# Kernel optimization log

Measured on AMD Instinct MI355X. Metric: run time of the kernel, lower is better.

## Reference

```python
import jax, jax.numpy as jnp
import numpy as np

N, K, CIN, COUT = 150000, 27, 32, 64
EPS = 1e-5
NEG_SLOPE = 0.01


def setup_inputs() -> dict:
    key = jax.random.key(0)
    k1, k2, k3, k4, k5, k6 = jax.random.split(key, 6)
    feats = jax.random.normal(k1, (N, CIN), dtype=jnp.float32)
    nbr = jax.random.randint(k2, (N, K), 0, N, dtype=jnp.int32)
    mask = jax.random.randint(k3, (N, K), 0, 2, dtype=jnp.int32).astype(jnp.bool_)
    # per-offset conv weights [K, Cin, Cout], kaiming-ish scale
    W = jax.random.normal(k4, (K, CIN, COUT), dtype=jnp.float32) / np.sqrt(K * CIN)
    gamma = jax.random.normal(k5, (COUT,), dtype=jnp.float32) * 0.1 + 1.0
    beta = jax.random.normal(k6, (COUT,), dtype=jnp.float32) * 0.1
    return {"feats": feats, "W": W, "gamma": gamma, "beta": beta, "nbr": nbr, "mask": mask}


def reference(feats, W, gamma, beta, nbr, mask):
    # sparse conv as gather-GEMM-(implicit scatter): out[n] = sum_k W[k]^T f[nbr[n,k]]
    gathered = jnp.where(mask[..., None], feats[nbr], 0.0)          # [N, K, Cin]
    out = jnp.einsum('nkc,kcd->nd', gathered, W)                     # [N, Cout]
    # BatchNorm over voxel axis (training-mode batch stats)
    mean = jnp.mean(out, axis=0)
    var = jnp.var(out, axis=0)
    out = (out - mean) * jax.lax.rsqrt(var + EPS) * gamma + beta
    # LeakyReLU, negative_slope = 0.01
    return jnp.where(out >= 0, out, NEG_SLOPE * out)
```

## Files before the change

### kernel.cpp

```cpp
#include <hip/hip_runtime.h>

#define N_VOX  150000
#define KNBR   27
#define CIN    32
#define COUT   64
#define NBUCKET 64
#define NEG_SLOPE 0.01f
#define EPS 1e-5f

typedef __bf16 bf16x8 __attribute__((ext_vector_type(8)));
typedef float  f32x4  __attribute__((ext_vector_type(4)));


__global__ __launch_bounds__(256) void prepack_feats(
    const float* __restrict__ f, __bf16* __restrict__ fb)
{
    const int i = blockIdx.x * 256 + threadIdx.x;
    if (i >= N_VOX * CIN / 8) return;
    const float4* p = reinterpret_cast<const float4*>(f) + (size_t)i * 2;
    const float4 a = p[0], b = p[1];
    bf16x8 o;
    o[0] = (__bf16)a.x; o[1] = (__bf16)a.y; o[2] = (__bf16)a.z; o[3] = (__bf16)a.w;
    o[4] = (__bf16)b.x; o[5] = (__bf16)b.y; o[6] = (__bf16)b.z; o[7] = (__bf16)b.w;
    reinterpret_cast<bf16x8*>(fb)[i] = o;
}

__global__ __launch_bounds__(256) void prepack_w(
    const float* __restrict__ W, __bf16* __restrict__ Wp)
{
    const int u = blockIdx.x * 256 + threadIdx.x;
    if (u >= KNBR * 4 * 64) return;
    const int lane = u & 63, f = u >> 6;
    const int s = f & 3, k = f >> 2;
    const int n = lane & 15, q = lane >> 4;
    const float* src = W + ((size_t)(k * CIN + q * 8) * COUT + s * 16 + n);
    bf16x8 o;
#pragma unroll
    for (int j = 0; j < 8; ++j) o[j] = (__bf16)src[(size_t)j * COUT];
    reinterpret_cast<bf16x8*>(Wp)[u] = o;
}

__global__ __launch_bounds__(256) void conv_mfma(
    const __bf16* __restrict__ fb,
    const __bf16* __restrict__ Wp,
    const int* __restrict__ nbr,
    const int* __restrict__ mask,
    float* __restrict__ out,
    float* __restrict__ bsums)
{
    const int t    = threadIdx.x;
    const int wave = t >> 6;
    const int lane = t & 63;
    const int n16  = lane & 15;
    const int q    = lane >> 4;
    const int arow = blockIdx.x * 64 + wave * 16 + n16;
    const bool rowok = arow < N_VOX;
    const size_t nb = rowok ? (size_t)arow * KNBR : 0;

    const bf16x8* __restrict__ bp = reinterpret_cast<const bf16x8*>(Wp);
    const bf16x8 zv = {};

    f32x4 acc0 = {0.f, 0.f, 0.f, 0.f};
    f32x4 acc1 = {0.f, 0.f, 0.f, 0.f};
    f32x4 acc2 = {0.f, 0.f, 0.f, 0.f};
    f32x4 acc3 = {0.f, 0.f, 0.f, 0.f};

#pragma unroll 3
    for (int k = 0; k < KNBR; ++k) {
        const int  mk = mask[nb + k];
        const int  ix = nbr[nb + k];
        const bool v  = rowok && (mk != 0);
        const int  ie = v ? ix : 0;
        bf16x8 a = *reinterpret_cast<const bf16x8*>(fb + (size_t)ie * CIN + q * 8);
        if (!v) a = zv;
        const bf16x8 b0 = bp[(k * 4 + 0) * 64 + lane];
        const bf16x8 b1 = bp[(k * 4 + 1) * 64 + lane];
        const bf16x8 b2 = bp[(k * 4 + 2) * 64 + lane];
        const bf16x8 b3 = bp[(k * 4 + 3) * 64 + lane];
        acc0 = __builtin_amdgcn_mfma_f32_16x16x32_bf16(a, b0, acc0, 0, 0, 0);
        acc1 = __builtin_amdgcn_mfma_f32_16x16x32_bf16(a, b1, acc1, 0, 0, 0);
        acc2 = __builtin_amdgcn_mfma_f32_16x16x32_bf16(a, b2, acc2, 0, 0, 0);
        acc3 = __builtin_amdgcn_mfma_f32_16x16x32_bf16(a, b3, acc3, 0, 0, 0);
    }

    const int orow_base = blockIdx.x * 64 + wave * 16 + q * 4;
    f32x4 accs[4] = {acc0, acc1, acc2, acc3};
#pragma unroll
    for (int r = 0; r < 4; ++r) {
        const int orow = orow_base + r;
        if (orow < N_VOX) {
            float* dst = out + (size_t)orow * COUT + n16;
#pragma unroll
            for (int s = 0; s < 4; ++s) dst[s * 16] = accs[s][r];
        }
    }

    float* dstb = bsums + ((blockIdx.x * 4 + wave) & (NBUCKET - 1)) * (2 * COUT);
#pragma unroll
    for (int s = 0; s < 4; ++s) {
        float ps = accs[s][0] + accs[s][1] + accs[s][2] + accs[s][3];
        float pq = accs[s][0] * accs[s][0] + accs[s][1] * accs[s][1]
                 + accs[s][2] * accs[s][2] + accs[s][3] * accs[s][3];
        ps += __shfl_down(ps, 32); ps += __shfl_down(ps, 16);
        pq += __shfl_down(pq, 32); pq += __shfl_down(pq, 16);
        if (q == 0) {
            atomicAdd(dstb + s * 16 + n16, ps);
            atomicAdd(dstb + COUT + s * 16 + n16, pq);
        }
    }
}

#define TM 64
#define FS 68
__global__ __launch_bounds__(256) void conv_f32(
    const float* __restrict__ feats, const float* __restrict__ W,
    const int* __restrict__ nbr, const int* __restrict__ mask,
    float* __restrict__ out, float* __restrict__ bsums)
{
    __shared__ float f_s[CIN * FS];
    __shared__ float w_s[CIN * COUT];
    const int t = threadIdx.x;
    const int tx = t & 15, ty = t >> 4;
    const int base = blockIdx.x * TM;
    const int gr = t >> 2, cq = t & 3;
    const int n_g = base + gr;
    float acc[4][4];
#pragma unroll
    for (int i = 0; i < 4; ++i)
#pragma unroll
        for (int j = 0; j < 4; ++j) acc[i][j] = 0.0f;
    for (int k = 0; k < KNBR; ++k) {
        int idx = -1;
        if (n_g < N_VOX) {
            const long off = (long)n_g * KNBR + k;
            if (mask[off] != 0) idx = nbr[off];
        }
        float4 fa = make_float4(0.f, 0.f, 0.f, 0.f);
        float4 fbv = fa;
        if (idx >= 0) {
            const float4* fp = reinterpret_cast<const float4*>(feats + (long)idx * CIN + cq * 8);
            fa = fp[0]; fbv = fp[1];
        }
        const float4* wsrc = reinterpret_cast<const float4*>(W + (long)k * CIN * COUT + t * 8);
        const float4 wa = wsrc[0], wb = wsrc[1];
        __syncthreads();
        const int c0 = cq * 8;
        f_s[(c0 + 0) * FS + gr] = fa.x; f_s[(c0 + 1) * FS + gr] = fa.y;
        f_s[(c0 + 2) * FS + gr] = fa.z; f_s[(c0 + 3) * FS + gr] = fa.w;
        f_s[(c0 + 4) * FS + gr] = fbv.x; f_s[(c0 + 5) * FS + gr] = fbv.y;
        f_s[(c0 + 6) * FS + gr] = fbv.z; f_s[(c0 + 7) * FS + gr] = fbv.w;
        reinterpret_cast<float4*>(w_s + t * 8)[0] = wa;
        reinterpret_cast<float4*>(w_s + t * 8)[1] = wb;
        __syncthreads();
#pragma unroll
        for (int c = 0; c < CIN; ++c) {
            const float4 fv = *reinterpret_cast<const float4*>(&f_s[c * FS + ty * 4]);
            const float4 wv = *reinterpret_cast<const float4*>(&w_s[c * COUT + tx * 4]);
            const float fr[4] = {fv.x, fv.y, fv.z, fv.w};
            const float wr[4] = {wv.x, wv.y, wv.z, wv.w};
#pragma unroll
            for (int i = 0; i < 4; ++i)
#pragma unroll
                for (int j = 0; j < 4; ++j)
                    acc[i][j] = fmaf(fr[i], wr[j], acc[i][j]);
        }
    }
#pragma unroll
    for (int i = 0; i < 4; ++i) {
        const int n = base + ty * 4 + i;
        if (n < N_VOX)
            *reinterpret_cast<float4*>(out + (long)n * COUT + tx * 4) =
                make_float4(acc[i][0], acc[i][1], acc[i][2], acc[i][3]);
    }
    float psum[4], psq[4];
#pragma unroll
    for (int j = 0; j < 4; ++j) {
        psum[j] = acc[0][j] + acc[1][j] + acc[2][j] + acc[3][j];
        psq[j]  = acc[0][j] * acc[0][j] + acc[1][j] * acc[1][j]
                + acc[2][j] * acc[2][j] + acc[3][j] * acc[3][j];
    }
    __syncthreads();
    *reinterpret_cast<float4*>(&f_s[ty * 64 + tx * 4]) = make_float4(psum[0], psum[1], psum[2], psum[3]);
    *reinterpret_cast<float4*>(&w_s[ty * 64 + tx * 4]) = make_float4(psq[0], psq[1], psq[2], psq[3]);
    __syncthreads();
    if (t < COUT) {
        float s = 0.f, qq = 0.f;
#pragma unroll
        for (int g = 0; g < 16; ++g) { s += f_s[g * 64 + t]; qq += w_s[g * 64 + t]; }
        float* dst = bsums + (blockIdx.x & (NBUCKET - 1)) * (2 * COUT);
        atomicAdd(dst + t, s);
        atomicAdd(dst + COUT + t, qq);
    }
}

__global__ __launch_bounds__(64) void stats_kernel(
    const float* __restrict__ bsums, const float* __restrict__ gamma,
    const float* __restrict__ beta, float* __restrict__ ss)
{
    const int d = threadIdx.x;
    float s = 0.f, q = 0.f;
    for (int b = 0; b < NBUCKET; ++b) {
        s += bsums[b * (2 * COUT) + d];
        q += bsums[b * (2 * COUT) + COUT + d];
    }
    const float inv_n = 1.0f / (float)N_VOX;
    const float mean  = s * inv_n;
    const float var   = q * inv_n - mean * mean;
    const float scale = gamma[d] * rsqrtf(var + EPS);
    ss[d]        = scale;
    ss[COUT + d] = beta[d] - mean * scale;
}

__global__ __launch_bounds__(256) void bn_apply_kernel(
    float* __restrict__ out, const float* __restrict__ ss)
{
    const long i = (long)blockIdx.x * 256 + threadIdx.x;
    const long total4 = (long)N_VOX * COUT / 4;
    if (i >= total4) return;
    float4 v = reinterpret_cast<float4*>(out)[i];
    const int cg = (int)(i & 15);
    const float4 sc = reinterpret_cast<const float4*>(ss)[cg];
    const float4 sh = reinterpret_cast<const float4*>(ss + COUT)[cg];
    float x;
    x = fmaf(v.x, sc.x, sh.x); v.x = (x >= 0.f) ? x : NEG_SLOPE * x;
    x = fmaf(v.y, sc.y, sh.y); v.y = (x >= 0.f) ? x : NEG_SLOPE * x;
    x = fmaf(v.z, sc.z, sh.z); v.z = (x >= 0.f) ? x : NEG_SLOPE * x;
    x = fmaf(v.w, sc.w, sh.w); v.w = (x >= 0.f) ? x : NEG_SLOPE * x;
    reinterpret_cast<float4*>(out)[i] = v;
}

extern "C" void kernel_launch(void* const* d_in, const int* in_sizes, int n_in,
                              void* d_out, int out_size, void* d_ws, size_t ws_size,
                              hipStream_t stream) {
    const float* feats = (const float*)d_in[0];
    const float* W     = (const float*)d_in[1];
    const float* gamma = (const float*)d_in[2];
    const float* beta  = (const float*)d_in[3];
    const int* nbr     = (const int*)d_in[4];
    const int* mask    = (const int*)d_in[5];
    float* out = (float*)d_out;
    char* ws   = (char*)d_ws;

    const size_t fb_bytes = (size_t)N_VOX * CIN * sizeof(__bf16);
    const size_t wp_bytes = (size_t)KNBR * 4 * 64 * 8 * sizeof(__bf16);
    const size_t bs_bytes = (size_t)NBUCKET * 2 * COUT * sizeof(float);
    const size_t ss_bytes = (size_t)2 * COUT * sizeof(float);
    const long total4 = (long)N_VOX * COUT / 4;

    if (ws_size >= fb_bytes + wp_bytes + bs_bytes + ss_bytes) {
        __bf16* fb  = (__bf16*)ws;
        __bf16* Wp  = (__bf16*)(ws + fb_bytes);
        float* bsums = (float*)(ws + fb_bytes + wp_bytes);
        float* ss    = (float*)(ws + fb_bytes + wp_bytes + bs_bytes);
        hipMemsetAsync(bsums, 0, bs_bytes, stream);
        prepack_feats<<<(N_VOX * CIN / 8 + 255) / 256, 256, 0, stream>>>(feats, fb);
        prepack_w<<<(KNBR * 4 * 64 + 255) / 256, 256, 0, stream>>>(W, Wp);
        conv_mfma<<<(N_VOX + 63) / 64, 256, 0, stream>>>(fb, Wp, nbr, mask, out, bsums);
        stats_kernel<<<1, 64, 0, stream>>>(bsums, gamma, beta, ss);
        bn_apply_kernel<<<(int)((total4 + 255) / 256), 256, 0, stream>>>(out, ss);
    } else {
        float* bsums = (float*)ws;
        float* ss    = (float*)(ws + bs_bytes);
        hipMemsetAsync(bsums, 0, bs_bytes, stream);
        conv_f32<<<(N_VOX + TM - 1) / TM, 256, 0, stream>>>(feats, W, nbr, mask, out, bsums);
        stats_kernel<<<1, 64, 0, stream>>>(bsums, gamma, beta, ss);
        bn_apply_kernel<<<(int)((total4 + 255) / 256), 256, 0, stream>>>(out, ss);
    }
}
```

Baseline: 190.4 us.

## Fuse prep kernels and precompute transposed masked neighbor index table

```diff
diff --git a/kernel.cpp b/kernel.cpp
--- a/kernel.cpp
+++ b/kernel.cpp
@@ -11,40 +11,73 @@
 typedef __bf16 bf16x8 __attribute__((ext_vector_type(8)));
 typedef float  f32x4  __attribute__((ext_vector_type(4)));
 
-
-__global__ __launch_bounds__(256) void prepack_feats(
-    const float* __restrict__ f, __bf16* __restrict__ fb)
-{
-    const int i = blockIdx.x * 256 + threadIdx.x;
-    if (i >= N_VOX * CIN / 8) return;
-    const float4* p = reinterpret_cast<const float4*>(f) + (size_t)i * 2;
-    const float4 a = p[0], b = p[1];
-    bf16x8 o;
-    o[0] = (__bf16)a.x; o[1] = (__bf16)a.y; o[2] = (__bf16)a.z; o[3] = (__bf16)a.w;
-    o[4] = (__bf16)b.x; o[5] = (__bf16)b.y; o[6] = (__bf16)b.z; o[7] = (__bf16)b.w;
-    reinterpret_cast<bf16x8*>(fb)[i] = o;
-}
-
-__global__ __launch_bounds__(256) void prepack_w(
-    const float* __restrict__ W, __bf16* __restrict__ Wp)
-{
-    const int u = blockIdx.x * 256 + threadIdx.x;
-    if (u >= KNBR * 4 * 64) return;
-    const int lane = u & 63, f = u >> 6;
-    const int s = f & 3, k = f >> 2;
-    const int n = lane & 15, q = lane >> 4;
-    const float* src = W + ((size_t)(k * CIN + q * 8) * COUT + s * 16 + n);
-    bf16x8 o;
-#pragma unroll
-    for (int j = 0; j < 8; ++j) o[j] = (__bf16)src[(size_t)j * COUT];
-    reinterpret_cast<bf16x8*>(Wp)[u] = o;
-}
-
-__global__ __launch_bounds__(256) void conv_mfma(
+#define NB_FEATS 2344
+#define NB_IDX    586
+#define NB_W       27
+#define NB_Z       32
+
+__global__ __launch_bounds__(256) void prep_all(
+    const float* __restrict__ feats, const float* __restrict__ W,
+    const int* __restrict__ nbr, const int* __restrict__ mask,
+    __bf16* __restrict__ fb, __bf16* __restrict__ Wp,
+    int* __restrict__ idxt, float* __restrict__ bsums, int do_idx)
+{
+    const int t = threadIdx.x;
+    int b = blockIdx.x;
+
+    if (b < NB_FEATS) {
+        const int i = b * 256 + t;
+        if (i < N_VOX * CIN / 8) {
+            const float4* p = reinterpret_cast<const float4*>(feats) + (size_t)i * 2;
+            const float4 a = p[0], c = p[1];
+            bf16x8 o;
+            o[0]=(__bf16)a.x; o[1]=(__bf16)a.y; o[2]=(__bf16)a.z; o[3]=(__bf16)a.w;
+            o[4]=(__bf16)c.x; o[5]=(__bf16)c.y; o[6]=(__bf16)c.z; o[7]=(__bf16)c.w;
+            reinterpret_cast<bf16x8*>(fb)[i] = o;
+        }
+        return;
+    }
+    b -= NB_FEATS;
+
+    if (do_idx) {
+        if (b < NB_IDX) {
+            const int n = b * 256 + t;
+            if (n < N_VOX) {
+                const int* np = nbr + (size_t)n * KNBR;
+                const int* mp = mask + (size_t)n * KNBR;
+#pragma unroll
+                for (int k = 0; k < KNBR; ++k) {
+                    const int v = mp[k] ? np[k] : -1;
+                    idxt[(size_t)k * N_VOX + n] = v;
+                }
+            }
+            return;
+        }
+        b -= NB_IDX;
+    }
+
+    if (b < NB_W) {
+        const int u = b * 256 + t;
+        const int lane = u & 63, f = u >> 6;
+        const int s = f & 3, k = f >> 2;
+        const int n = lane & 15, q = lane >> 4;
+        const float* src = W + ((size_t)(k * CIN + q * 8) * COUT + s * 16 + n);
+        bf16x8 o;
+#pragma unroll
+        for (int j = 0; j < 8; ++j) o[j] = (__bf16)src[(size_t)j * COUT];
+        reinterpret_cast<bf16x8*>(Wp)[u] = o;
+        return;
+    }
+    b -= NB_W;
+
+    const int z = b * 256 + t;
+    if (z < NBUCKET * 2 * COUT) bsums[z] = 0.0f;
+}
+
+__global__ __launch_bounds__(256, 3) void conv_mfma2(
     const __bf16* __restrict__ fb,
     const __bf16* __restrict__ Wp,
-    const int* __restrict__ nbr,
-    const int* __restrict__ mask,
+    const int* __restrict__ idxt,
     float* __restrict__ out,
     float* __restrict__ bsums)
 {
@@ -55,22 +88,23 @@
     const int q    = lane >> 4;
     const int arow = blockIdx.x * 64 + wave * 16 + n16;
     const bool rowok = arow < N_VOX;
-    const size_t nb = rowok ? (size_t)arow * KNBR : 0;
+    const int arc = rowok ? arow : 0;
+
+    int idx[KNBR];
+#pragma unroll
+    for (int k = 0; k < KNBR; ++k)
+        idx[k] = rowok ? idxt[(size_t)k * N_VOX + arc] : -1;
 
     const bf16x8* __restrict__ bp = reinterpret_cast<const bf16x8*>(Wp);
     const bf16x8 zv = {};
 
-    f32x4 acc0 = {0.f, 0.f, 0.f, 0.f};
-    f32x4 acc1 = {0.f, 0.f, 0.f, 0.f};
-    f32x4 acc2 = {0.f, 0.f, 0.f, 0.f};
-    f32x4 acc3 = {0.f, 0.f, 0.f, 0.f};
-
-#pragma unroll 3
+    f32x4 acc0 = {0.f,0.f,0.f,0.f}, acc1 = {0.f,0.f,0.f,0.f};
+    f32x4 acc2 = {0.f,0.f,0.f,0.f}, acc3 = {0.f,0.f,0.f,0.f};
+
+#pragma unroll 9
     for (int k = 0; k < KNBR; ++k) {
-        const int  mk = mask[nb + k];
-        const int  ix = nbr[nb + k];
-        const bool v  = rowok && (mk != 0);
-        const int  ie = v ? ix : 0;
+        const bool v  = idx[k] >= 0;
+        const int  ie = v ? idx[k] : 0;
         bf16x8 a = *reinterpret_cast<const bf16x8*>(fb + (size_t)ie * CIN + q * 8);
         if (!v) a = zv;
         const bf16x8 b0 = bp[(k * 4 + 0) * 64 + lane];
@@ -110,86 +144,61 @@
     }
 }
 
-#define TM 64
-#define FS 68
-__global__ __launch_bounds__(256) void conv_f32(
-    const float* __restrict__ feats, const float* __restrict__ W,
+__global__ __launch_bounds__(256) void conv_mfma1(
+    const __bf16* __restrict__ fb, const __bf16* __restrict__ Wp,
     const int* __restrict__ nbr, const int* __restrict__ mask,
     float* __restrict__ out, float* __restrict__ bsums)
 {
-    __shared__ float f_s[CIN * FS];
-    __shared__ float w_s[CIN * COUT];
     const int t = threadIdx.x;
-    const int tx = t & 15, ty = t >> 4;
-    const int base = blockIdx.x * TM;
-    const int gr = t >> 2, cq = t & 3;
-    const int n_g = base + gr;
-    float acc[4][4];
-#pragma unroll
-    for (int i = 0; i < 4; ++i)
-#pragma unroll
-        for (int j = 0; j < 4; ++j) acc[i][j] = 0.0f;
+    const int wave = t >> 6, lane = t & 63;
+    const int n16 = lane & 15, q = lane >> 4;
+    const int arow = blockIdx.x * 64 + wave * 16 + n16;
+    const bool rowok = arow < N_VOX;
+    const size_t nb = rowok ? (size_t)arow * KNBR : 0;
+    const bf16x8* __restrict__ bp = reinterpret_cast<const bf16x8*>(Wp);
+    const bf16x8 zv = {};
+    f32x4 acc0 = {0.f,0.f,0.f,0.f}, acc1 = {0.f,0.f,0.f,0.f};
+    f32x4 acc2 = {0.f,0.f,0.f,0.f}, acc3 = {0.f,0.f,0.f,0.f};
+#pragma unroll 3
     for (int k = 0; k < KNBR; ++k) {
-        int idx = -1;
-        if (n_g < N_VOX) {
-            const long off = (long)n_g * KNBR + k;
-            if (mask[off] != 0) idx = nbr[off];
-        }
-        float4 fa = make_float4(0.f, 0.f, 0.f, 0.f);
-        float4 fbv = fa;
-        if (idx >= 0) {
-            const float4* fp = reinterpret_cast<const float4*>(feats + (long)idx * CIN + cq * 8);
-            fa = fp[0]; fbv = fp[1];
-        }
-        const float4* wsrc = reinterpret_cast<const float4*>(W + (long)k * CIN * COUT + t * 8);
-        const float4 wa = wsrc[0], wb = wsrc[1];
-        __syncthreads();
-        const int c0 = cq * 8;
-        f_s[(c0 + 0) * FS + gr] = fa.x; f_s[(c0 + 1) * FS + gr] = fa.y;
-        f_s[(c0 + 2) * FS + gr] = fa.z; f_s[(c0 + 3) * FS + gr] = fa.w;
-        f_s[(c0 + 4) * FS + gr] = fbv.x; f_s[(c0 + 5) * FS + gr] = fbv.y;
-        f_s[(c0 + 6) * FS + gr] = fbv.z; f_s[(c0 + 7) * FS + gr] = fbv.w;
-        reinterpret_cast<float4*>(w_s + t * 8)[0] = wa;
-        reinterpret_cast<float4*>(w_s + t * 8)[1] = wb;
-        __syncthreads();
-#pragma unroll
-        for (int c = 0; c < CIN; ++c) {
-            const float4 fv = *reinterpret_cast<const float4*>(&f_s[c * FS + ty * 4]);
-            const float4 wv = *reinterpret_cast<const float4*>(&w_s[c * COUT + tx * 4]);
-            const float fr[4] = {fv.x, fv.y, fv.z, fv.w};
-            const float wr[4] = {wv.x, wv.y, wv.z, wv.w};
-#pragma unroll
-            for (int i = 0; i < 4; ++i)
-#pragma unroll
-                for (int j = 0; j < 4; ++j)
-                    acc[i][j] = fmaf(fr[i], wr[j], acc[i][j]);
-        }
-    }
-#pragma unroll
-    for (int i = 0; i < 4; ++i) {
-        const int n = base + ty * 4 + i;
-        if (n < N_VOX)
-            *reinterpret_cast<float4*>(out + (long)n * COUT + tx * 4) =
-                make_float4(acc[i][0], acc[i][1], acc[i][2], acc[i][3]);
-    }
-    float psum[4], psq[4];
-#pragma unroll
-    for (int j = 0; j < 4; ++j) {
-        psum[j] = acc[0][j] + acc[1][j] + acc[2][j] + acc[3][j];
-        psq[j]  = acc[0][j] * acc[0][j] + acc[1][j] * acc[1][j]
-                + acc[2][j] * acc[2][j] + acc[3][j] * acc[3][j];
-    }
-    __syncthreads();
-    *reinterpret_cast<float4*>(&f_s[ty * 64 + tx * 4]) = make_float4(psum[0], psum[1], psum[2], psum[3]);
-    *reinterpret_cast<float4*>(&w_s[ty * 64 + tx * 4]) = make_float4(psq[0], psq[1], psq[2], psq[3]);
-    __syncthreads();
-    if (t < COUT) {
-        float s = 0.f, qq = 0.f;
-#pragma unroll
-        for (int g = 0; g < 16; ++g) { s += f_s[g * 64 + t]; qq += w_s[g * 64 + t]; }
-        float* dst = bsums + (blockIdx.x & (NBUCKET - 1)) * (2 * COUT);
-        atomicAdd(dst + t, s);
-        atomicAdd(dst + COUT + t, qq);
+        const int mk = mask[nb + k];
+        const int ix = nbr[nb + k];
+        const bool v = rowok && (mk != 0);
+        const int ie = v ? ix : 0;
+        bf16x8 a = *reinterpret_cast<const bf16x8*>(fb + (size_t)ie * CIN + q * 8);
+        if (!v) a = zv;
+        const bf16x8 b0 = bp[(k * 4 + 0) * 64 + lane];
+        const bf16x8 b1 = bp[(k * 4 + 1) * 64 + lane];
+        const bf16x8 b2 = bp[(k * 4 + 2) * 64 + lane];
+        const bf16x8 b3 = bp[(k * 4 + 3) * 64 + lane];
+        acc0 = __builtin_amdgcn_mfma_f32_16x16x32_bf16(a, b0, acc0, 0, 0, 0);
+        acc1 = __builtin_amdgcn_mfma_f32_16x16x32_bf16(a, b1, acc1, 0, 0, 0);
+        acc2 = __builtin_amdgcn_mfma_f32_16x16x32_bf16(a, b2, acc2, 0, 0, 0);
+        acc3 = __builtin_amdgcn_mfma_f32_16x16x32_bf16(a, b3, acc3, 0, 0, 0);
+    }
+    const int orow_base = blockIdx.x * 64 + wave * 16 + q * 4;
+    f32x4 accs[4] = {acc0, acc1, acc2, acc3};
+#pragma unroll
+    for (int r = 0; r < 4; ++r) {
+        const int orow = orow_base + r;
+        if (orow < N_VOX) {
+            float* dst = out + (size_t)orow * COUT + n16;
+#pragma unroll
+            for (int s = 0; s < 4; ++s) dst[s * 16] = accs[s][r];
+        }
+    }
+    float* dstb = bsums + ((blockIdx.x * 4 + wave) & (NBUCKET - 1)) * (2 * COUT);
+#pragma unroll
+    for (int s = 0; s < 4; ++s) {
+        float ps = accs[s][0] + accs[s][1] + accs[s][2] + accs[s][3];
+        float pq = accs[s][0] * accs[s][0] + accs[s][1] * accs[s][1]
+                 + accs[s][2] * accs[s][2] + accs[s][3] * accs[s][3];
+        ps += __shfl_down(ps, 32); ps += __shfl_down(ps, 16);
+        pq += __shfl_down(pq, 32); pq += __shfl_down(pq, 16);
+        if (q == 0) {
+            atomicAdd(dstb + s * 16 + n16, ps);
+            atomicAdd(dstb + COUT + s * 16 + n16, pq);
+        }
     }
 }
 
@@ -241,29 +250,34 @@
     float* out = (float*)d_out;
     char* ws   = (char*)d_ws;
 
-    const size_t fb_bytes = (size_t)N_VOX * CIN * sizeof(__bf16);
-    const size_t wp_bytes = (size_t)KNBR * 4 * 64 * 8 * sizeof(__bf16);
-    const size_t bs_bytes = (size_t)NBUCKET * 2 * COUT * sizeof(float);
-    const size_t ss_bytes = (size_t)2 * COUT * sizeof(float);
+    const size_t fb_bytes  = (size_t)N_VOX * CIN * sizeof(__bf16);
+    const size_t wp_bytes  = (size_t)KNBR * 4 * 64 * 8 * sizeof(__bf16);
+    const size_t idx_bytes = (size_t)KNBR * N_VOX * sizeof(int);
+    const size_t bs_bytes  = (size_t)NBUCKET * 2 * COUT * sizeof(float);
+    const size_t ss_bytes  = (size_t)2 * COUT * sizeof(float);
     const long total4 = (long)N_VOX * COUT / 4;
-
-    if (ws_size >= fb_bytes + wp_bytes + bs_bytes + ss_bytes) {
-        __bf16* fb  = (__bf16*)ws;
-        __bf16* Wp  = (__bf16*)(ws + fb_bytes);
+    const int apply_blocks = (int)((total4 + 255) / 256);
+    const int conv_blocks  = (N_VOX + 63) / 64;
+
+    __bf16* fb = (__bf16*)ws;
+    __bf16* Wp = (__bf16*)(ws + fb_bytes);
+
+    if (ws_size >= fb_bytes + wp_bytes + idx_bytes + bs_bytes + ss_bytes) {
+        int*   idxt  = (int*)(ws + fb_bytes + wp_bytes);
+        float* bsums = (float*)(ws + fb_bytes + wp_bytes + idx_bytes);
+        float* ss    = (float*)(ws + fb_bytes + wp_bytes + idx_bytes + bs_bytes);
+        prep_all<<<NB_FEATS + NB_IDX + NB_W + NB_Z, 256, 0, stream>>>(
+            feats, W, nbr, mask, fb, Wp, idxt, bsums, 1);
+        conv_mfma2<<<conv_blocks, 256, 0, stream>>>(fb, Wp, idxt, out, bsums);
+        stats_kernel<<<1, 64, 0, stream>>>(bsums, gamma, beta, ss);
+        bn_apply_kernel<<<apply_blocks, 256, 0, stream>>>(out, ss);
+    } else {
         float* bsums = (float*)(ws + fb_bytes + wp_bytes);
         float* ss    = (float*)(ws + fb_bytes + wp_bytes + bs_bytes);
-        hipMemsetAsync(bsums, 0, bs_bytes, stream);
-        prepack_feats<<<(N_VOX * CIN / 8 + 255) / 256, 256, 0, stream>>>(feats, fb);
-        prepack_w<<<(KNBR * 4 * 64 + 255) / 256, 256, 0, stream>>>(W, Wp);
-        conv_mfma<<<(N_VOX + 63) / 64, 256, 0, stream>>>(fb, Wp, nbr, mask, out, bsums);
+        prep_all<<<NB_FEATS + NB_W + NB_Z, 256, 0, stream>>>(
+            feats, W, nbr, mask, fb, Wp, nullptr, bsums, 0);
+        conv_mfma1<<<conv_blocks, 256, 0, stream>>>(fb, Wp, nbr, mask, out, bsums);
         stats_kernel<<<1, 64, 0, stream>>>(bsums, gamma, beta, ss);
-        bn_apply_kernel<<<(int)((total4 + 255) / 256), 256, 0, stream>>>(out, ss);
-    } else {
-        float* bsums = (float*)ws;
-        float* ss    = (float*)(ws + bs_bytes);
-        hipMemsetAsync(bsums, 0, bs_bytes, stream);
-        conv_f32<<<(N_VOX + TM - 1) / TM, 256, 0, stream>>>(feats, W, nbr, mask, out, bsums);
-        stats_kernel<<<1, 64, 0, stream>>>(bsums, gamma, beta, ss);
-        bn_apply_kernel<<<(int)((total4 + 255) / 256), 256, 0, stream>>>(out, ss);
-    }
-}
+        bn_apply_kernel<<<apply_blocks, 256, 0, stream>>>(out, ss);
+    }
+}
```

Measured after the change: 228.5 us. +20.0%, slower.

## Fuse prep kernels and memset, prefetch neighbor indices, merge BN stats into apply

Applied to the files above, without the earlier changes.

```diff
diff --git a/kernel.cpp b/kernel.cpp
--- a/kernel.cpp
+++ b/kernel.cpp
@@ -7,40 +7,56 @@
 #define NBUCKET 64
 #define NEG_SLOPE 0.01f
 #define EPS 1e-5f
+#define APPLY_BLOCKS 1024
 
 typedef __bf16 bf16x8 __attribute__((ext_vector_type(8)));
 typedef float  f32x4  __attribute__((ext_vector_type(4)));
 
-
-__global__ __launch_bounds__(256) void prepack_feats(
-    const float* __restrict__ f, __bf16* __restrict__ fb)
-{
-    const int i = blockIdx.x * 256 + threadIdx.x;
-    if (i >= N_VOX * CIN / 8) return;
-    const float4* p = reinterpret_cast<const float4*>(f) + (size_t)i * 2;
-    const float4 a = p[0], b = p[1];
-    bf16x8 o;
-    o[0] = (__bf16)a.x; o[1] = (__bf16)a.y; o[2] = (__bf16)a.z; o[3] = (__bf16)a.w;
-    o[4] = (__bf16)b.x; o[5] = (__bf16)b.y; o[6] = (__bf16)b.z; o[7] = (__bf16)b.w;
-    reinterpret_cast<bf16x8*>(fb)[i] = o;
-}
-
-__global__ __launch_bounds__(256) void prepack_w(
-    const float* __restrict__ W, __bf16* __restrict__ Wp)
-{
-    const int u = blockIdx.x * 256 + threadIdx.x;
-    if (u >= KNBR * 4 * 64) return;
-    const int lane = u & 63, f = u >> 6;
-    const int s = f & 3, k = f >> 2;
-    const int n = lane & 15, q = lane >> 4;
-    const float* src = W + ((size_t)(k * CIN + q * 8) * COUT + s * 16 + n);
-    bf16x8 o;
-#pragma unroll
-    for (int j = 0; j < 8; ++j) o[j] = (__bf16)src[(size_t)j * COUT];
-    reinterpret_cast<bf16x8*>(Wp)[u] = o;
-}
-
-__global__ __launch_bounds__(256) void conv_mfma(
+#define NB_FEATS 2344
+#define NB_W       27
+#define NB_Z       32
+
+__global__ __launch_bounds__(256) void prep_all(
+    const float* __restrict__ feats, const float* __restrict__ W,
+    __bf16* __restrict__ fb, __bf16* __restrict__ Wp,
+    float* __restrict__ bsums)
+{
+    const int t = threadIdx.x;
+    int b = blockIdx.x;
+
+    if (b < NB_FEATS) {
+        const int i = b * 256 + t;
+        if (i < N_VOX * CIN / 8) {
+            const float4* p = reinterpret_cast<const float4*>(feats) + (size_t)i * 2;
+            const float4 a = p[0], c = p[1];
+            bf16x8 o;
+            o[0]=(__bf16)a.x; o[1]=(__bf16)a.y; o[2]=(__bf16)a.z; o[3]=(__bf16)a.w;
+            o[4]=(__bf16)c.x; o[5]=(__bf16)c.y; o[6]=(__bf16)c.z; o[7]=(__bf16)c.w;
+            reinterpret_cast<bf16x8*>(fb)[i] = o;
+        }
+        return;
+    }
+    b -= NB_FEATS;
+
+    if (b < NB_W) {
+        const int u = b * 256 + t;
+        const int lane = u & 63, f = u >> 6;
+        const int s = f & 3, k = f >> 2;
+        const int n = lane & 15, q = lane >> 4;
+        const float* src = W + ((size_t)(k * CIN + q * 8) * COUT + s * 16 + n);
+        bf16x8 o;
+#pragma unroll
+        for (int j = 0; j < 8; ++j) o[j] = (__bf16)src[(size_t)j * COUT];
+        reinterpret_cast<bf16x8*>(Wp)[u] = o;
+        return;
+    }
+    b -= NB_W;
+
+    const int z = b * 256 + t;
+    if (z < NBUCKET * 2 * COUT) bsums[z] = 0.0f;
+}
+
+__global__ __launch_bounds__(256, 3) void conv_mfma3(
     const __bf16* __restrict__ fb,
     const __bf16* __restrict__ Wp,
     const int* __restrict__ nbr,
@@ -55,22 +71,26 @@
     const int q    = lane >> 4;
     const int arow = blockIdx.x * 64 + wave * 16 + n16;
     const bool rowok = arow < N_VOX;
-    const size_t nb = rowok ? (size_t)arow * KNBR : 0;
+    const size_t nb = (size_t)(rowok ? arow : 0) * KNBR;
+
+    int idx[KNBR];
+#pragma unroll
+    for (int k = 0; k < KNBR; ++k) {
+        const int m  = mask[nb + k];
+        const int ix = nbr[nb + k];
+        idx[k] = (rowok && m != 0) ? ix : -1;
+    }
 
     const bf16x8* __restrict__ bp = reinterpret_cast<const bf16x8*>(Wp);
     const bf16x8 zv = {};
 
-    f32x4 acc0 = {0.f, 0.f, 0.f, 0.f};
-    f32x4 acc1 = {0.f, 0.f, 0.f, 0.f};
-    f32x4 acc2 = {0.f, 0.f, 0.f, 0.f};
-    f32x4 acc3 = {0.f, 0.f, 0.f, 0.f};
-
-#pragma unroll 3
+    f32x4 acc0 = {0.f,0.f,0.f,0.f}, acc1 = {0.f,0.f,0.f,0.f};
+    f32x4 acc2 = {0.f,0.f,0.f,0.f}, acc3 = {0.f,0.f,0.f,0.f};
+
+#pragma unroll 9
     for (int k = 0; k < KNBR; ++k) {
-        const int  mk = mask[nb + k];
-        const int  ix = nbr[nb + k];
-        const bool v  = rowok && (mk != 0);
-        const int  ie = v ? ix : 0;
+        const bool v  = idx[k] >= 0;
+        const int  ie = v ? idx[k] : 0;
         bf16x8 a = *reinterpret_cast<const bf16x8*>(fb + (size_t)ie * CIN + q * 8);
         if (!v) a = zv;
         const bf16x8 b0 = bp[(k * 4 + 0) * 64 + lane];
@@ -107,6 +127,45 @@
             atomicAdd(dstb + s * 16 + n16, ps);
             atomicAdd(dstb + COUT + s * 16 + n16, pq);
         }
+    }
+}
+
+__global__ __launch_bounds__(256) void bn_stats_apply(
+    float* __restrict__ out, const float* __restrict__ bsums,
+    const float* __restrict__ gamma, const float* __restrict__ beta)
+{
+    __shared__ float s_sc[COUT], s_sh[COUT];
+    const int t = threadIdx.x;
+    if (t < COUT) {
+        float s = 0.f, qq = 0.f;
+#pragma unroll 8
+        for (int b = 0; b < NBUCKET; ++b) {
+            s  += bsums[b * (2 * COUT) + t];
+            qq += bsums[b * (2 * COUT) + COUT + t];
+        }
+        const float inv_n = 1.0f / (float)N_VOX;
+        const float mean  = s * inv_n;
+        const float var   = qq * inv_n - mean * mean;
+        const float scale = gamma[t] * rsqrtf(var + EPS);
+        s_sc[t] = scale;
+        s_sh[t] = beta[t] - mean * scale;
+    }
+    __syncthreads();
+
+    const long total4 = (long)N_VOX * COUT / 4;
+    const long stride = (long)APPLY_BLOCKS * 256;
+    long i = (long)blockIdx.x * 256 + t;
+    const int cg = (int)(i & 15);
+    const float4 sc = reinterpret_cast<const float4*>(s_sc)[cg];
+    const float4 sh = reinterpret_cast<const float4*>(s_sh)[cg];
+    for (; i < total4; i += stride) {
+        float4 v = reinterpret_cast<float4*>(out)[i];
+        float x;
+        x = fmaf(v.x, sc.x, sh.x); v.x = (x >= 0.f) ? x : NEG_SLOPE * x;
+        x = fmaf(v.y, sc.y, sh.y); v.y = (x >= 0.f) ? x : NEG_SLOPE * x;
+        x = fmaf(v.z, sc.z, sh.z); v.z = (x >= 0.f) ? x : NEG_SLOPE * x;
+        x = fmaf(v.w, sc.w, sh.w); v.w = (x >= 0.f) ? x : NEG_SLOPE * x;
+        reinterpret_cast<float4*>(out)[i] = v;
     }
 }
 
@@ -193,42 +252,6 @@
     }
 }
 
-__global__ __launch_bounds__(64) void stats_kernel(
-    const float* __restrict__ bsums, const float* __restrict__ gamma,
-    const float* __restrict__ beta, float* __restrict__ ss)
-{
-    const int d = threadIdx.x;
-    float s = 0.f, q = 0.f;
-    for (int b = 0; b < NBUCKET; ++b) {
-        s += bsums[b * (2 * COUT) + d];
-        q += bsums[b * (2 * COUT) + COUT + d];
-    }
-    const float inv_n = 1.0f / (float)N_VOX;
-    const float mean  = s * inv_n;
-    const float var   = q * inv_n - mean * mean;
-    const float scale = gamma[d] * rsqrtf(var + EPS);
-    ss[d]        = scale;
-    ss[COUT + d] = beta[d] - mean * scale;
-}
-
-__global__ __launch_bounds__(256) void bn_apply_kernel(
-    float* __restrict__ out, const float* __restrict__ ss)
-{
-    const long i = (long)blockIdx.x * 256 + threadIdx.x;
-    const long total4 = (long)N_VOX * COUT / 4;
-    if (i >= total4) return;
-    float4 v = reinterpret_cast<float4*>(out)[i];
-    const int cg = (int)(i & 15);
-    const float4 sc = reinterpret_cast<const float4*>(ss)[cg];
-    const float4 sh = reinterpret_cast<const float4*>(ss + COUT)[cg];
-    float x;
-    x = fmaf(v.x, sc.x, sh.x); v.x = (x >= 0.f) ? x : NEG_SLOPE * x;
-    x = fmaf(v.y, sc.y, sh.y); v.y = (x >= 0.f) ? x : NEG_SLOPE * x;
-    x = fmaf(v.z, sc.z, sh.z); v.z = (x >= 0.f) ? x : NEG_SLOPE * x;
-    x = fmaf(v.w, sc.w, sh.w); v.w = (x >= 0.f) ? x : NEG_SLOPE * x;
-    reinterpret_cast<float4*>(out)[i] = v;
-}
-
 extern "C" void kernel_launch(void* const* d_in, const int* in_sizes, int n_in,
                               void* d_out, int out_size, void* d_ws, size_t ws_size,
                               hipStream_t stream) {
@@ -244,26 +267,19 @@
     const size_t fb_bytes = (size_t)N_VOX * CIN * sizeof(__bf16);
     const size_t wp_bytes = (size_t)KNBR * 4 * 64 * 8 * sizeof(__bf16);
     const size_t bs_bytes = (size_t)NBUCKET * 2 * COUT * sizeof(float);
-    const size_t ss_bytes = (size_t)2 * COUT * sizeof(float);
-    const long total4 = (long)N_VOX * COUT / 4;
-
-    if (ws_size >= fb_bytes + wp_bytes + bs_bytes + ss_bytes) {
-        __bf16* fb  = (__bf16*)ws;
-        __bf16* Wp  = (__bf16*)(ws + fb_bytes);
+    const int conv_blocks = (N_VOX + 63) / 64;
+
+    if (ws_size >= fb_bytes + wp_bytes + bs_bytes) {
+        __bf16* fb   = (__bf16*)ws;
+        __bf16* Wp   = (__bf16*)(ws + fb_bytes);
         float* bsums = (float*)(ws + fb_bytes + wp_bytes);
-        float* ss    = (float*)(ws + fb_bytes + wp_bytes + bs_bytes);
-        hipMemsetAsync(bsums, 0, bs_bytes, stream);
-        prepack_feats<<<(N_VOX * CIN / 8 + 255) / 256, 256, 0, stream>>>(feats, fb);
-        prepack_w<<<(KNBR * 4 * 64 + 255) / 256, 256, 0, stream>>>(W, Wp);
-        conv_mfma<<<(N_VOX + 63) / 64, 256, 0, stream>>>(fb, Wp, nbr, mask, out, bsums);
-        stats_kernel<<<1, 64, 0, stream>>>(bsums, gamma, beta, ss);
-        bn_apply_kernel<<<(int)((total4 + 255) / 256), 256, 0, stream>>>(out, ss);
+        prep_all<<<NB_FEATS + NB_W + NB_Z, 256, 0, stream>>>(feats, W, fb, Wp, bsums);
+        conv_mfma3<<<conv_blocks, 256, 0, stream>>>(fb, Wp, nbr, mask, out, bsums);
+        bn_stats_apply<<<APPLY_BLOCKS, 256, 0, stream>>>(out, bsums, gamma, beta);
     } else {
         float* bsums = (float*)ws;
-        float* ss    = (float*)(ws + bs_bytes);
         hipMemsetAsync(bsums, 0, bs_bytes, stream);
         conv_f32<<<(N_VOX + TM - 1) / TM, 256, 0, stream>>>(feats, W, nbr, mask, out, bsums);
-        stats_kernel<<<1, 64, 0, stream>>>(bsums, gamma, beta, ss);
-        bn_apply_kernel<<<(int)((total4 + 255) / 256), 256, 0, stream>>>(out, ss);
-    }
-}
+        bn_stats_apply<<<APPLY_BLOCKS, 256, 0, stream>>>(out, bsums, gamma, beta);
+    }
+}
```

Result: faster. 179.3 us (-5.8%).
